# Optimization experiments

Hardware: AMD Instinct MI355X
Metric: run time of the kernel (lower is better)

## Reference

```python
import jax, jax.numpy as jnp
import numpy as np

B, I, H = 256, 512, 512


def _lin_init(k, out_dim, in_dim):
    bound = 1.0 / np.sqrt(in_dim)
    kw, kb = jax.random.split(k)
    W = jax.random.uniform(kw, (out_dim, in_dim), minval=-bound, maxval=bound, dtype=jnp.float32)
    b = jax.random.uniform(kb, (out_dim,), minval=-bound, maxval=bound, dtype=jnp.float32)
    return W, b


def setup_inputs() -> dict:
    key = jax.random.key(0)
    ks = jax.random.split(key, 16)
    inp = {}
    inp['inputs'] = jax.random.normal(ks[0], (B, I), dtype=jnp.float32)
    inp['h0'] = jax.random.normal(ks[1], (B, H), dtype=jnp.float32) * 0.1
    inp['c0'] = jax.random.normal(ks[2], (B, H), dtype=jnp.float32) * 0.1
    inp['hebb'] = jax.random.uniform(ks[3], (B, H, H), minval=-0.01, maxval=0.01, dtype=jnp.float32)
    # plastic recurrent weights: w = 0.02*rand - 0.01, alpha = 1e-4*rand
    inp['w'] = 0.02 * jax.random.uniform(ks[4], (H, H), dtype=jnp.float32) - 0.01
    inp['alpha'] = 1e-4 * jax.random.uniform(ks[5], (1, 1, H), dtype=jnp.float32)
    inp['Wxf'], inp['bxf'] = _lin_init(ks[6], H, I)
    inp['Whf'], inp['bhf'] = _lin_init(ks[7], H, H)
    inp['Wxi'], inp['bxi'] = _lin_init(ks[8], H, I)
    inp['Whi'], inp['bhi'] = _lin_init(ks[9], H, H)
    inp['Wxo'], inp['bxo'] = _lin_init(ks[10], H, I)
    inp['Who'], inp['bho'] = _lin_init(ks[11], H, H)
    inp['Wxc'], inp['bxc'] = _lin_init(ks[12], H, I)
    inp['Wmod'], inp['bmod'] = _lin_init(ks[13], 1, H)   # h2mod: H -> 1
    inp['Wfan'], inp['bfan'] = _lin_init(ks[14], H, 1)   # modfanout: 1 -> H
    return inp


def reference(inputs, h0, c0, hebb, w, alpha,
              Wxf, bxf, Whf, bhf, Wxi, bxi, Whi, bhi,
              Wxo, bxo, Who, bho, Wxc, bxc, Wmod, bmod, Wfan, bfan):
    # gates (torch Linear: y = x @ W.T + b)
    fgt = jax.nn.sigmoid(inputs @ Wxf.T + bxf + h0 @ Whf.T + bhf)
    ipt = jax.nn.sigmoid(inputs @ Wxi.T + bxi + h0 @ Whi.T + bhi)
    opt = jax.nn.sigmoid(inputs @ Wxo.T + bxo + h0 @ Who.T + bho)
    # plastic recurrent path: h0 @ (w + alpha * hebb), per-sample fast weights
    h2c = jnp.einsum('bh,bhk->bk', h0, w + alpha * hebb)
    inputstocell = jnp.tanh(inputs @ Wxc.T + bxc + h2c)
    cell = fgt * c0 + ipt * inputstocell
    hactiv = opt * jnp.tanh(cell)
    # Hebbian outer-product trace update with neuromodulated learning rate
    deltahebb = jnp.einsum('bh,bk->bhk', h0, inputstocell)  # [B,H,H]
    myeta = jnp.tanh(hactiv @ Wmod.T + bmod)                # [B,1]
    myeta = myeta * Wfan[:, 0][None, :] + bfan              # modfanout(1->H): [B,H]
    hebb_new = jnp.clip(hebb + myeta[:, None, :] * deltahebb, -2.0, 2.0)
    return hactiv, cell, hebb_new
```

## Files before the change

### kernel.cpp

```cpp
#include <hip/hip_runtime.h>
#include <math.h>

#define B_ 256
#define I_ 512
#define H_ 512
#define BH (B_*H_)

typedef float f4v __attribute__((ext_vector_type(4)));


#define TK 32
#define LDB 34
#define TILE_F (TK*LDB)
#define NGEMM 1024

__global__ __launch_bounds__(256) void k_gates(
    const float* __restrict__ h0, const float* __restrict__ inputs,
    const float* __restrict__ Wxf, const float* __restrict__ Whf,
    const float* __restrict__ Wxi, const float* __restrict__ Whi,
    const float* __restrict__ Wxo, const float* __restrict__ Who,
    const float* __restrict__ Wxc, const float* __restrict__ w,
    float* __restrict__ pre) {

    __shared__ float smem[4 * TILE_F];
    int bid = blockIdx.x;
    int tid = threadIdx.x;

    int ks = bid & 1;
    int m0 = ((bid >> 1) & 7) * 32;
    int n0 = (bid >> 4) * 32;
    int g  = n0 >> 9;
    int ko0 = n0 & 511;

    const float* Asrc = ks ? h0 : inputs;
    const float* Bsrc;
    bool wpath = false;
    if (ks == 0) {
        Bsrc = (g == 0) ? Wxf : (g == 1) ? Wxi : (g == 2) ? Wxo : Wxc;
    } else {
        if (g == 3) { Bsrc = w; wpath = true; }
        else Bsrc = (g == 0) ? Whf : (g == 1) ? Whi : Who;
    }

    int row = tid >> 3;
    int c4  = tid & 7;
    int tx  = tid & 15, ty = tid >> 4;

    float acc[2][2] = {{0.f, 0.f}, {0.f, 0.f}};
    float4 areg, breg;

    auto LOAD = [&](int t) {
        int kb = t * TK;
        areg = *(const float4*)&Asrc[(size_t)(m0 + row) * 512 + kb + c4 * 4];
        if (wpath)
            breg = *(const float4*)&Bsrc[(size_t)(kb + row) * 512 + ko0 + c4 * 4];
        else
            breg = *(const float4*)&Bsrc[(size_t)(ko0 + row) * 512 + kb + c4 * 4];
    };
    auto STORE = [&](int pbuf) {
        float* As = smem + pbuf * 2 * TILE_F;
        float* Bs = As + TILE_F;
        #pragma unroll
        for (int j = 0; j < 4; ++j)
            As[(c4 * 4 + j) * LDB + row] = ((const float*)&areg)[j];
        if (wpath) {
            #pragma unroll
            for (int j = 0; j < 4; ++j)
                Bs[row * LDB + c4 * 4 + j] = ((const float*)&breg)[j];
        } else {
            #pragma unroll
            for (int j = 0; j < 4; ++j)
                Bs[(c4 * 4 + j) * LDB + row] = ((const float*)&breg)[j];
        }
    };

    LOAD(0);
    STORE(0);
    for (int t = 0; t < 16; ++t) {
        __syncthreads();
        if (t < 15) LOAD(t + 1);
        int pb = t & 1;
        const float* As = smem + pb * 2 * TILE_F;
        const float* Bs = As + TILE_F;
        #pragma unroll
        for (int kk = 0; kk < TK; ++kk) {
            float2 a2 = *(const float2*)&As[kk * LDB + ty * 2];
            float2 b2 = *(const float2*)&Bs[kk * LDB + tx * 2];
            acc[0][0] += a2.x * b2.x; acc[0][1] += a2.x * b2.y;
            acc[1][0] += a2.y * b2.x; acc[1][1] += a2.y * b2.y;
        }
        if (t < 15) STORE(pb ^ 1);
    }

    float* pb_out = pre + (size_t)(ks * 4 + g) * BH;
    #pragma unroll
    for (int i = 0; i < 2; ++i) {
        #pragma unroll
        for (int j = 0; j < 2; ++j) {
            int bnum = m0 + ty * 2 + i;
            int ko = ko0 + tx * 2 + j;
            pb_out[(size_t)bnum * H_ + ko] = acc[i][j];
        }
    }
}

__global__ __launch_bounds__(512) void k_dotfin(
    const float* __restrict__ hebb, const float* __restrict__ h0,
    const float* __restrict__ pre, const float* __restrict__ c0,
    const float* __restrict__ alpha,
    const float* __restrict__ bxf, const float* __restrict__ bhf,
    const float* __restrict__ bxi, const float* __restrict__ bhi,
    const float* __restrict__ bxo, const float* __restrict__ bho,
    const float* __restrict__ bxc,
    const float* __restrict__ Wmod, const float* __restrict__ bmod,
    const float* __restrict__ Wfan, const float* __restrict__ bfan,
    float* __restrict__ out, float* __restrict__ v) {

    __shared__ float h0s[H_];
    __shared__ float plds[4 * H_];
    __shared__ float red[8];

    int b = blockIdx.x;
    int t = threadIdx.x;

    h0s[t & 511] = h0[(size_t)b * H_ + (t & 511)];
    __syncthreads();

    int hg = t >> 7;
    int k4 = t & 127;
    const float4* hb4 = (const float4*)hebb + ((size_t)b << 16);
    float4 acc = make_float4(0.f, 0.f, 0.f, 0.f);
    #pragma unroll 8
    for (int r = 0; r < 128; ++r) {
        int h = (hg << 7) + r;
        float s = h0s[h];
        float4 vv = hb4[(size_t)h * 128 + k4];
        acc.x += s * vv.x; acc.y += s * vv.y;
        acc.z += s * vv.z; acc.w += s * vv.w;
    }
    ((float4*)plds)[hg * 128 + k4] = acc;
    __syncthreads();

    int k = t;
    float dot = plds[k] + plds[H_ + k] + plds[2 * H_ + k] + plds[3 * H_ + k];
    size_t off = (size_t)b * H_ + k;
    float pf = pre[0 * BH + off] + pre[4 * BH + off] + bxf[k] + bhf[k];
    float pi = pre[1 * BH + off] + pre[5 * BH + off] + bxi[k] + bhi[k];
    float po = pre[2 * BH + off] + pre[6 * BH + off] + bxo[k] + bho[k];
    float pc = pre[3 * BH + off] + pre[7 * BH + off] + bxc[k];
    float c2 = tanhf(pc + alpha[k] * dot);
    float fg = 1.f / (1.f + expf(-pf));
    float ig = 1.f / (1.f + expf(-pi));
    float og = 1.f / (1.f + expf(-po));
    float cell = fg * c0[off] + ig * c2;
    float ha = og * tanhf(cell);
    out[off] = ha;
    out[BH + off] = cell;

    float x = ha * Wmod[k];
    #pragma unroll
    for (int o = 32; o > 0; o >>= 1) x += __shfl_down(x, o, 64);
    int wid = t >> 6, lane = t & 63;
    if (lane == 0) red[wid] = x;
    __syncthreads();
    float s8 = red[0] + red[1] + red[2] + red[3]
             + red[4] + red[5] + red[6] + red[7];
    float myeta = tanhf(s8 + bmod[0]);
    v[off] = (myeta * Wfan[k] + bfan[k]) * c2;
}

__global__ __launch_bounds__(256) void k_update(
    const float4* __restrict__ hebb, const float* __restrict__ h0,
    const float* __restrict__ v, float* __restrict__ out) {
    const int total = B_ * H_ * (H_ / 4);
    int stride = gridDim.x * blockDim.x;
    int base = blockIdx.x * blockDim.x + threadIdx.x;
    for (int f = total - stride + base; f >= 0; f -= stride) {
        int k4 = f & 127;
        int h  = (f >> 7) & 511;
        int b  = f >> 16;
        float u = h0[(b << 9) + h];
        const float4* vv4 = (const float4*)v;
        float4 vv = vv4[(b << 7) + k4];
        float4 hb = hebb[f];
        f4v r;
        r.x = fminf(fmaxf(hb.x + u * vv.x, -2.f), 2.f);
        r.y = fminf(fmaxf(hb.y + u * vv.y, -2.f), 2.f);
        r.z = fminf(fmaxf(hb.z + u * vv.z, -2.f), 2.f);
        r.w = fminf(fmaxf(hb.w + u * vv.w, -2.f), 2.f);
        __builtin_nontemporal_store(r, (f4v*)(out) + f);
    }
}

extern "C" void kernel_launch(void* const* d_in, const int* in_sizes, int n_in,
                              void* d_out, int out_size, void* d_ws, size_t ws_size,
                              hipStream_t stream) {
    const float* inputs = (const float*)d_in[0];
    const float* h0     = (const float*)d_in[1];
    const float* c0     = (const float*)d_in[2];
    const float* hebb   = (const float*)d_in[3];
    const float* w      = (const float*)d_in[4];
    const float* alpha  = (const float*)d_in[5];
    const float* Wxf = (const float*)d_in[6];  const float* bxf = (const float*)d_in[7];
    const float* Whf = (const float*)d_in[8];  const float* bhf = (const float*)d_in[9];
    const float* Wxi = (const float*)d_in[10]; const float* bxi = (const float*)d_in[11];
    const float* Whi = (const float*)d_in[12]; const float* bhi = (const float*)d_in[13];
    const float* Wxo = (const float*)d_in[14]; const float* bxo = (const float*)d_in[15];
    const float* Who = (const float*)d_in[16]; const float* bho = (const float*)d_in[17];
    const float* Wxc = (const float*)d_in[18]; const float* bxc = (const float*)d_in[19];
    const float* Wmod = (const float*)d_in[20]; const float* bmod = (const float*)d_in[21];
    const float* Wfan = (const float*)d_in[22]; const float* bfan = (const float*)d_in[23];

    float* out = (float*)d_out;
    float* ws  = (float*)d_ws;
    float* pre  = ws;
    float* vbuf = ws + 8 * BH;

    k_gates<<<NGEMM, 256, 0, stream>>>(h0, inputs,
        Wxf, Whf, Wxi, Whi, Wxo, Who, Wxc, w, pre);
    k_dotfin<<<B_, 512, 0, stream>>>(hebb, h0, pre, c0, alpha,
        bxf, bhf, bxi, bhi, bxo, bho, bxc,
        Wmod, bmod, Wfan, bfan, out, vbuf);
    k_update<<<2048, 256, 0, stream>>>((const float4*)hebb, h0, vbuf,
                                       out + 2 * BH);
}
```

Baseline: 189.5 us.

## Replace FP32 gate GEMM with split-bf16 MFMA GEMM over concatenated K

Adds a conversion kernel that packs [inputs|h0] and the stacked gate weights (with w transposed) into hi/lo bf16 pairs. The gate GEMM then runs on MFMA 16x16x32 bf16 using three products (hi·hi, hi·lo, lo·hi) to approximate FP32 accuracy. Concatenating K removes the split-K partial outputs, and the biases are folded into the GEMM epilogue, so dotfin reads 4 pre-activation planes instead of 8. The cost is an extra conversion pass on every call, a fourth launch, and GEMM operands read directly from global memory without LDS staging.

```diff
diff --git a/kernel.cpp b/kernel.cpp
--- a/kernel.cpp
+++ b/kernel.cpp
@@ -1,106 +1,104 @@
 #include <hip/hip_runtime.h>
+#include <hip/hip_bf16.h>
 #include <math.h>
 
 #define B_ 256
 #define I_ 512
 #define H_ 512
 #define BH (B_*H_)
-
-typedef float f4v __attribute__((ext_vector_type(4)));
-
-
-#define TK 32
-#define LDB 34
-#define TILE_F (TK*LDB)
-#define NGEMM 1024
-
-__global__ __launch_bounds__(256) void k_gates(
-    const float* __restrict__ h0, const float* __restrict__ inputs,
+#define KA 1024
+
+typedef float f4v  __attribute__((ext_vector_type(4)));
+typedef short s8v  __attribute__((ext_vector_type(8)));
+typedef float f32x4 __attribute__((ext_vector_type(4)));
+
+
+#define A_ELEMS (256*1024)
+#define B_ELEMS (2048*1024)
+
+__global__ __launch_bounds__(256) void k_convert(
+    const float* __restrict__ inputs, const float* __restrict__ h0,
     const float* __restrict__ Wxf, const float* __restrict__ Whf,
     const float* __restrict__ Wxi, const float* __restrict__ Whi,
     const float* __restrict__ Wxo, const float* __restrict__ Who,
     const float* __restrict__ Wxc, const float* __restrict__ w,
+    ushort* __restrict__ Ahi, ushort* __restrict__ Alo,
+    ushort* __restrict__ Bhi, ushort* __restrict__ Blo) {
+    const int NTOT = A_ELEMS + B_ELEMS;
+    int stride = gridDim.x * blockDim.x;
+    for (int f = blockIdx.x * blockDim.x + threadIdx.x; f < NTOT; f += stride) {
+        float x; ushort* dhi; ushort* dlo; int idx;
+        if (f < A_ELEMS) {
+            idx = f;
+            int m = f >> 10, k = f & 1023;
+            x = (k < 512) ? inputs[m * 512 + k] : h0[m * 512 + (k - 512)];
+            dhi = Ahi; dlo = Alo;
+        } else {
+            idx = f - A_ELEMS;
+            int n = idx >> 10, k = idx & 1023;
+            int g = n >> 9, ko = n & 511;
+            if (k < 512) {
+                const float* W = (g == 0) ? Wxf : (g == 1) ? Wxi : (g == 2) ? Wxo : Wxc;
+                x = W[ko * 512 + k];
+            } else if (g < 3) {
+                const float* W = (g == 0) ? Whf : (g == 1) ? Whi : Who;
+                x = W[ko * 512 + (k - 512)];
+            } else {
+                x = w[(size_t)(k - 512) * 512 + ko];
+            }
+            dhi = Bhi; dlo = Blo;
+        }
+        __hip_bfloat16 h = __float2bfloat16(x);
+        float hf = __bfloat162float(h);
+        __hip_bfloat16 l = __float2bfloat16(x - hf);
+        dhi[idx] = *(ushort*)&h;
+        dlo[idx] = *(ushort*)&l;
+    }
+}
+
+__global__ __launch_bounds__(256) void k_mfma_gates(
+    const ushort* __restrict__ Ahi, const ushort* __restrict__ Alo,
+    const ushort* __restrict__ Bhi, const ushort* __restrict__ Blo,
+    const float* __restrict__ bxf, const float* __restrict__ bhf,
+    const float* __restrict__ bxi, const float* __restrict__ bhi,
+    const float* __restrict__ bxo, const float* __restrict__ bho,
+    const float* __restrict__ bxc,
     float* __restrict__ pre) {
-
-    __shared__ float smem[4 * TILE_F];
-    int bid = blockIdx.x;
-    int tid = threadIdx.x;
-
-    int ks = bid & 1;
-    int m0 = ((bid >> 1) & 7) * 32;
-    int n0 = (bid >> 4) * 32;
+    int wave = threadIdx.x >> 6, lane = threadIdx.x & 63;
+    int tile = blockIdx.x * 4 + wave;
+    int m0 = (tile & 15) << 4;
+    int n0 = (tile >> 4) << 4;
+    int r  = lane & 15;
+    int kg = lane >> 4;
+
+    const s8v* pa_hi = (const s8v*)(Ahi + (size_t)(m0 + r) * KA + kg * 8);
+    const s8v* pa_lo = (const s8v*)(Alo + (size_t)(m0 + r) * KA + kg * 8);
+    const s8v* pb_hi = (const s8v*)(Bhi + (size_t)(n0 + r) * KA + kg * 8);
+    const s8v* pb_lo = (const s8v*)(Blo + (size_t)(n0 + r) * KA + kg * 8);
+
+    f32x4 acc = {0.f, 0.f, 0.f, 0.f};
+    #pragma unroll 4
+    for (int kc = 0; kc < 32; ++kc) {
+        s8v ah = pa_hi[kc * 4];
+        s8v al = pa_lo[kc * 4];
+        s8v bh = pb_hi[kc * 4];
+        s8v bl = pb_lo[kc * 4];
+        acc = __builtin_amdgcn_mfma_f32_16x16x32_bf16(ah, bh, acc, 0, 0, 0);
+        acc = __builtin_amdgcn_mfma_f32_16x16x32_bf16(ah, bl, acc, 0, 0, 0);
+        acc = __builtin_amdgcn_mfma_f32_16x16x32_bf16(al, bh, acc, 0, 0, 0);
+    }
+
     int g  = n0 >> 9;
-    int ko0 = n0 & 511;
-
-    const float* Asrc = ks ? h0 : inputs;
-    const float* Bsrc;
-    bool wpath = false;
-    if (ks == 0) {
-        Bsrc = (g == 0) ? Wxf : (g == 1) ? Wxi : (g == 2) ? Wxo : Wxc;
-    } else {
-        if (g == 3) { Bsrc = w; wpath = true; }
-        else Bsrc = (g == 0) ? Whf : (g == 1) ? Whi : Who;
-    }
-
-    int row = tid >> 3;
-    int c4  = tid & 7;
-    int tx  = tid & 15, ty = tid >> 4;
-
-    float acc[2][2] = {{0.f, 0.f}, {0.f, 0.f}};
-    float4 areg, breg;
-
-    auto LOAD = [&](int t) {
-        int kb = t * TK;
-        areg = *(const float4*)&Asrc[(size_t)(m0 + row) * 512 + kb + c4 * 4];
-        if (wpath)
-            breg = *(const float4*)&Bsrc[(size_t)(kb + row) * 512 + ko0 + c4 * 4];
-        else
-            breg = *(const float4*)&Bsrc[(size_t)(ko0 + row) * 512 + kb + c4 * 4];
-    };
-    auto STORE = [&](int pbuf) {
-        float* As = smem + pbuf * 2 * TILE_F;
-        float* Bs = As + TILE_F;
-        #pragma unroll
-        for (int j = 0; j < 4; ++j)
-            As[(c4 * 4 + j) * LDB + row] = ((const float*)&areg)[j];
-        if (wpath) {
-            #pragma unroll
-            for (int j = 0; j < 4; ++j)
-                Bs[row * LDB + c4 * 4 + j] = ((const float*)&breg)[j];
-        } else {
-            #pragma unroll
-            for (int j = 0; j < 4; ++j)
-                Bs[(c4 * 4 + j) * LDB + row] = ((const float*)&breg)[j];
-        }
-    };
-
-    LOAD(0);
-    STORE(0);
-    for (int t = 0; t < 16; ++t) {
-        __syncthreads();
-        if (t < 15) LOAD(t + 1);
-        int pb = t & 1;
-        const float* As = smem + pb * 2 * TILE_F;
-        const float* Bs = As + TILE_F;
-        #pragma unroll
-        for (int kk = 0; kk < TK; ++kk) {
-            float2 a2 = *(const float2*)&As[kk * LDB + ty * 2];
-            float2 b2 = *(const float2*)&Bs[kk * LDB + tx * 2];
-            acc[0][0] += a2.x * b2.x; acc[0][1] += a2.x * b2.y;
-            acc[1][0] += a2.y * b2.x; acc[1][1] += a2.y * b2.y;
-        }
-        if (t < 15) STORE(pb ^ 1);
-    }
-
-    float* pb_out = pre + (size_t)(ks * 4 + g) * BH;
+    int ko = (n0 & 511) + r;
+    float bias;
+    if (g == 0)      bias = bxf[ko] + bhf[ko];
+    else if (g == 1) bias = bxi[ko] + bhi[ko];
+    else if (g == 2) bias = bxo[ko] + bho[ko];
+    else             bias = bxc[ko];
     #pragma unroll
-    for (int i = 0; i < 2; ++i) {
-        #pragma unroll
-        for (int j = 0; j < 2; ++j) {
-            int bnum = m0 + ty * 2 + i;
-            int ko = ko0 + tx * 2 + j;
-            pb_out[(size_t)bnum * H_ + ko] = acc[i][j];
-        }
+    for (int j = 0; j < 4; ++j) {
+        int m = m0 + kg * 4 + j;
+        pre[(size_t)g * BH + (size_t)m * H_ + ko] = acc[j] + bias;
     }
 }
 
@@ -108,10 +106,6 @@
     const float* __restrict__ hebb, const float* __restrict__ h0,
     const float* __restrict__ pre, const float* __restrict__ c0,
     const float* __restrict__ alpha,
-    const float* __restrict__ bxf, const float* __restrict__ bhf,
-    const float* __restrict__ bxi, const float* __restrict__ bhi,
-    const float* __restrict__ bxo, const float* __restrict__ bho,
-    const float* __restrict__ bxc,
     const float* __restrict__ Wmod, const float* __restrict__ bmod,
     const float* __restrict__ Wfan, const float* __restrict__ bfan,
     float* __restrict__ out, float* __restrict__ v) {
@@ -144,10 +138,10 @@
     int k = t;
     float dot = plds[k] + plds[H_ + k] + plds[2 * H_ + k] + plds[3 * H_ + k];
     size_t off = (size_t)b * H_ + k;
-    float pf = pre[0 * BH + off] + pre[4 * BH + off] + bxf[k] + bhf[k];
-    float pi = pre[1 * BH + off] + pre[5 * BH + off] + bxi[k] + bhi[k];
-    float po = pre[2 * BH + off] + pre[6 * BH + off] + bxo[k] + bho[k];
-    float pc = pre[3 * BH + off] + pre[7 * BH + off] + bxc[k];
+    float pf = pre[0 * BH + off];
+    float pi = pre[1 * BH + off];
+    float po = pre[2 * BH + off];
+    float pc = pre[3 * BH + off];
     float c2 = tanhf(pc + alpha[k] * dot);
     float fg = 1.f / (1.f + expf(-pf));
     float ig = 1.f / (1.f + expf(-pi));
@@ -213,13 +207,18 @@
 
     float* out = (float*)d_out;
     float* ws  = (float*)d_ws;
-    float* pre  = ws;
-    float* vbuf = ws + 8 * BH;
-
-    k_gates<<<NGEMM, 256, 0, stream>>>(h0, inputs,
-        Wxf, Whf, Wxi, Whi, Wxo, Who, Wxc, w, pre);
+    float*  pre  = ws;
+    float*  vbuf = ws + 4 * BH;
+    ushort* Ahi  = (ushort*)(ws + 5 * BH);
+    ushort* Alo  = Ahi + A_ELEMS;
+    ushort* Bhi  = Alo + A_ELEMS;
+    ushort* Blo  = Bhi + B_ELEMS;
+
+    k_convert<<<2048, 256, 0, stream>>>(inputs, h0,
+        Wxf, Whf, Wxi, Whi, Wxo, Who, Wxc, w, Ahi, Alo, Bhi, Blo);
+    k_mfma_gates<<<512, 256, 0, stream>>>(Ahi, Alo, Bhi, Blo,
+        bxf, bhf, bxi, bhi, bxo, bho, bxc, pre);
     k_dotfin<<<B_, 512, 0, stream>>>(hebb, h0, pre, c0, alpha,
-        bxf, bhf, bxi, bhi, bxo, bho, bxc,
         Wmod, bmod, Wfan, bfan, out, vbuf);
     k_update<<<2048, 256, 0, stream>>>((const float4*)hebb, h0, vbuf,
                                        out + 2 * BH);
```

New measurement: 189.0 us. Within noise of the previous version (-0.3%).
